# Kernel tuning notes

Measured on AMD Instinct MI355X. Metric: run time of the kernel, lower is better.

The kernel has to match this reference:

```python
import jax, jax.numpy as jnp
import numpy as np

HEADS = 8
LANDMARKS = 256   # dim // 2
PINV_ITERS = 6
CONV_K = 33       # residual_conv_kernel default in NystromAttention
N_BOTTLENECKS = 4
DIM = 512


def layer_norm(x, w, b, eps=1e-5):
    mu = jnp.mean(x, -1, keepdims=True)
    xc = x - mu
    var = jnp.mean(xc * xc, -1, keepdims=True)
    return xc * jax.lax.rsqrt(var + eps) * w + b


def moore_penrose_pinv(x, iters=PINV_ITERS):
    # faithful to lucidrains: global max over row/col sums
    col = jnp.abs(x).sum(-1).max()
    row = jnp.abs(x).sum(-2).max()
    z = jnp.swapaxes(x, -1, -2) / (col * row)
    I = jnp.eye(x.shape[-1], dtype=x.dtype)
    for _ in range(iters):
        xz = x @ z
        z = 0.25 * z @ (13.0 * I - xz @ (15.0 * I - xz @ (7.0 * I - xz)))
    return z


def nystrom_attention(x, qkv_w, out_w, out_b, conv_w):
    b, n, d = x.shape
    m = LANDMARKS
    pad = (-n) % m
    x = jnp.pad(x, ((0, 0), (pad, 0), (0, 0)))  # pad at FRONT of seq, like F.pad
    N = n + pad
    dh = d // HEADS  # 64
    qkv = x @ qkv_w.T                      # (b, N, 3*d)
    q, k, v = jnp.split(qkv, 3, axis=-1)

    def heads(t):
        return t.reshape(b, N, HEADS, dh).transpose(0, 2, 1, 3)  # (b, h, N, dh)

    q, k, v = heads(q), heads(k), heads(v)
    q = q * (dh ** -0.5)
    l = N // m
    # einops reduce '... (n l) d -> ... n d' sum, then / l
    q_l = q.reshape(b, HEADS, m, l, dh).sum(3) / l
    k_l = k.reshape(b, HEADS, m, l, dh).sum(3) / l
    attn1 = jax.nn.softmax(jnp.einsum('bhid,bhjd->bhij', q, k_l), -1)    # (b,h,N,m)
    attn2 = jax.nn.softmax(jnp.einsum('bhid,bhjd->bhij', q_l, k_l), -1)  # (b,h,m,m)
    attn3 = jax.nn.softmax(jnp.einsum('bhid,bhjd->bhij', q_l, k), -1)    # (b,h,m,N)
    attn2_inv = moore_penrose_pinv(attn2)
    out = (attn1 @ attn2_inv) @ (attn3 @ v)  # (b,h,N,dh)
    # residual depthwise conv over seq dim, per head (groups=heads, bias=False)
    res = jax.lax.conv_general_dilated(
        v, conv_w, window_strides=(1, 1),
        padding=((CONV_K // 2, CONV_K // 2), (0, 0)),
        dimension_numbers=('NCHW', 'OIHW', 'NCHW'),
        feature_group_count=HEADS)
    out = out + res
    out = out.transpose(0, 2, 1, 3).reshape(b, N, d)
    out = out @ out_w.T + out_b  # to_out (dropout is identity in eval)
    return out[:, -n:]


def trans_layer(x, ln_w, ln_b, qkv_w, out_w, out_b, conv_w, omega):
    h = layer_norm(x, ln_w, ln_b)
    a = nystrom_attention(h, qkv_w, out_w, out_b, conv_w)
    # torch: `attn_output, *_ = attn(...)` strips batch dim then broadcasts;
    # with b==1 this equals the plain admin residual below.
    return x * omega + a


def setup_inputs() -> dict:
    key = jax.random.key(0)
    ks = jax.random.split(key, 20)
    d = DIM
    s = 1.0 / np.sqrt(d)
    inp = {
        'x1': jax.random.normal(ks[0], (1, 16384, d), jnp.float32),
        'x2': jax.random.normal(ks[1], (1, 2048, d), jnp.float32),
        'bottleneck': jax.random.uniform(ks[2], (1, N_BOTTLENECKS, d), jnp.float32),
    }
    for i, base in ((1, 3), (2, 10)):
        inp[f'ln{i}_w'] = jnp.ones((d,), jnp.float32)
        inp[f'ln{i}_b'] = jnp.zeros((d,), jnp.float32)
        inp[f'qkv{i}_w'] = jax.random.normal(ks[base], (3 * d, d), jnp.float32) * s
        inp[f'out{i}_w'] = jax.random.normal(ks[base + 1], (d, d), jnp.float32) * s
        inp[f'out{i}_b'] = jnp.zeros((d,), jnp.float32)
        inp[f'conv{i}_w'] = jax.random.normal(ks[base + 2], (HEADS, 1, CONV_K, 1), jnp.float32) * (1.0 / np.sqrt(CONV_K))
        inp[f'omega{i}'] = jnp.full((1,), np.sqrt(8.0), jnp.float32)  # admin_torch.as_module(8)
    return inp


def reference(x1, x2, bottleneck,
              ln1_w, ln1_b, qkv1_w, out1_w, out1_b, conv1_w, omega1,
              ln2_w, ln2_b, qkv2_w, out2_w, out2_b, conv2_w, omega2):
    seq = x1.shape[1]
    bn = jnp.concatenate([bottleneck, x2], axis=1)
    bn = trans_layer(bn, ln2_w, ln2_b, qkv2_w, out2_w, out2_b, conv2_w, omega2)
    bn = bn[:, :N_BOTTLENECKS, :]
    x = jnp.concatenate([x1, bn], axis=1)
    x = trans_layer(x, ln1_w, ln1_b, qkv1_w, out1_w, out1_b, conv1_w, omega1)
    return x[:, :seq, :]
```

## Files before the change

kernel.cpp:

```cpp
#include <hip/hip_runtime.h>
#include <math.h>

#define QKVLD 1536

__global__ __launch_bounds__(256) void ln_pad_kernel(
    const float* __restrict__ src1, int n1,
    const float* __restrict__ src2,
    const float* __restrict__ w, const float* __restrict__ b,
    float* __restrict__ h, int pad)
{
    int r = blockIdx.x;
    int tid = threadIdx.x;
    float* out = h + (size_t)r * 512;
    if (r < pad) { out[tid] = 0.f; out[tid + 256] = 0.f; return; }
    int i = r - pad;
    const float* src = (i < n1) ? (src1 + (size_t)i * 512)
                                : (src2 + (size_t)(i - n1) * 512);
    float x0 = src[tid], x1 = src[tid + 256];
    float s = x0 + x1, sq = x0 * x0 + x1 * x1;
#pragma unroll
    for (int o = 32; o >= 1; o >>= 1) { s += __shfl_xor(s, o); sq += __shfl_xor(sq, o); }
    __shared__ float rs[4], rq[4];
    int wid = tid >> 6, lane = tid & 63;
    if (lane == 0) { rs[wid] = s; rq[wid] = sq; }
    __syncthreads();
    s = rs[0] + rs[1] + rs[2] + rs[3];
    sq = rq[0] + rq[1] + rq[2] + rq[3];
    float mu = s * (1.f / 512.f);
    float var = sq * (1.f / 512.f) - mu * mu;
    float inv = rsqrtf(var + 1e-5f);
    out[tid]       = (x0 - mu) * inv * w[tid] + b[tid];
    out[tid + 256] = (x1 - mu) * inv * w[tid + 256] + b[tid + 256];
}

__global__ __launch_bounds__(256) void gemm_nt128(
    const float* __restrict__ A, const float* __restrict__ B, float* __restrict__ C,
    int K, int lda, int ldb, int ldc,
    const float* __restrict__ resid, const float* __restrict__ bias,
    const float* __restrict__ omega)
{
    __shared__ __align__(16) float As[16][128];
    __shared__ __align__(16) float Bs[16][128];
    int tid = threadIdx.x;
    int tx = tid & 15, ty = tid >> 4;
    int row0 = blockIdx.x * 128, col0 = blockIdx.y * 128;
    int lr = tid >> 1, lk = (tid & 1) << 3;
    const float* Ap = A + (size_t)(row0 + lr) * lda + lk;
    const float* Bp = B + (size_t)(col0 + lr) * ldb + lk;
    float acc[8][8] = {};
    float4 a0 = *(const float4*)(Ap);
    float4 a1 = *(const float4*)(Ap + 4);
    float4 b0 = *(const float4*)(Bp);
    float4 b1 = *(const float4*)(Bp + 4);
    for (int kt = 0; kt < K; kt += 16) {
        __syncthreads();
        As[lk + 0][lr] = a0.x; As[lk + 1][lr] = a0.y; As[lk + 2][lr] = a0.z; As[lk + 3][lr] = a0.w;
        As[lk + 4][lr] = a1.x; As[lk + 5][lr] = a1.y; As[lk + 6][lr] = a1.z; As[lk + 7][lr] = a1.w;
        Bs[lk + 0][lr] = b0.x; Bs[lk + 1][lr] = b0.y; Bs[lk + 2][lr] = b0.z; Bs[lk + 3][lr] = b0.w;
        Bs[lk + 4][lr] = b1.x; Bs[lk + 5][lr] = b1.y; Bs[lk + 6][lr] = b1.z; Bs[lk + 7][lr] = b1.w;
        __syncthreads();
        if (kt + 16 < K) {
            a0 = *(const float4*)(Ap + kt + 16); a1 = *(const float4*)(Ap + kt + 20);
            b0 = *(const float4*)(Bp + kt + 16); b1 = *(const float4*)(Bp + kt + 20);
        }
#pragma unroll
        for (int k = 0; k < 16; ++k) {
            float4 av0 = *(const float4*)(&As[k][ty << 2]);
            float4 av1 = *(const float4*)(&As[k][64 + (ty << 2)]);
            float4 bv0 = *(const float4*)(&Bs[k][tx << 2]);
            float4 bv1 = *(const float4*)(&Bs[k][64 + (tx << 2)]);
            float a[8] = {av0.x, av0.y, av0.z, av0.w, av1.x, av1.y, av1.z, av1.w};
            float bb[8] = {bv0.x, bv0.y, bv0.z, bv0.w, bv1.x, bv1.y, bv1.z, bv1.w};
#pragma unroll
            for (int i = 0; i < 8; ++i)
#pragma unroll
                for (int j = 0; j < 8; ++j) acc[i][j] += a[i] * bb[j];
        }
    }
#pragma unroll
    for (int ih = 0; ih < 2; ++ih)
#pragma unroll
    for (int i = 0; i < 4; ++i) {
        int r = row0 + ih * 64 + (ty << 2) + i;
#pragma unroll
        for (int jh = 0; jh < 2; ++jh) {
            int c = col0 + jh * 64 + (tx << 2);
            float4 o = make_float4(acc[ih * 4 + i][jh * 4 + 0], acc[ih * 4 + i][jh * 4 + 1],
                                   acc[ih * 4 + i][jh * 4 + 2], acc[ih * 4 + i][jh * 4 + 3]);
            if (resid) {
                float om = omega[0];
                float4 rv = *(const float4*)(resid + (size_t)r * ldc + c);
                float4 bv = *(const float4*)(bias + c);
                o.x += om * rv.x + bv.x; o.y += om * rv.y + bv.y;
                o.z += om * rv.z + bv.z; o.w += om * rv.w + bv.w;
            }
            *(float4*)(C + (size_t)r * ldc + c) = o;
        }
    }
}

__global__ __launch_bounds__(256) void landmarks_kernel(
    const float* __restrict__ qkv, float* __restrict__ ql, float* __restrict__ kl, int l)
{
    int j = blockIdx.x;
    int tid = threadIdx.x;
    float inv = 1.f / (float)l;
    const float* base = qkv + (size_t)j * l * QKVLD;
    float sq0 = 0, sq1 = 0, sk0 = 0, sk1 = 0;
    for (int r = 0; r < l; ++r) {
        const float* row = base + (size_t)r * QKVLD;
        sq0 += row[tid]; sq1 += row[tid + 256];
        sk0 += row[512 + tid]; sk1 += row[512 + tid + 256];
    }
    ql[j * 512 + tid] = sq0 * inv; ql[j * 512 + tid + 256] = sq1 * inv;
    kl[j * 512 + tid] = sk0 * inv; kl[j * 512 + tid + 256] = sk1 * inv;
}

__global__ __launch_bounds__(256) void attn2_kernel(
    const float* __restrict__ ql, const float* __restrict__ kl, float* __restrict__ a2)
{
    int hh = blockIdx.y, i = blockIdx.x;
    int tid = threadIdx.x;
    __shared__ float qrow[64];
    __shared__ float red[4], red2[4];
    if (tid < 64) qrow[tid] = 0.125f * ql[i * 512 + hh * 64 + tid];
    __syncthreads();
    const float* krow = kl + (size_t)tid * 512 + hh * 64;
    float sc = 0.f;
#pragma unroll
    for (int d = 0; d < 64; ++d) sc += qrow[d] * krow[d];
    float m = sc;
#pragma unroll
    for (int o = 32; o >= 1; o >>= 1) m = fmaxf(m, __shfl_xor(m, o));
    int wid = tid >> 6, lane = tid & 63;
    if (lane == 0) red[wid] = m;
    __syncthreads();
    m = fmaxf(fmaxf(red[0], red[1]), fmaxf(red[2], red[3]));
    float p = __expf(sc - m);
    float s = p;
#pragma unroll
    for (int o = 32; o >= 1; o >>= 1) s += __shfl_xor(s, o);
    if (lane == 0) red2[wid] = s;
    __syncthreads();
    s = red2[0] + red2[1] + red2[2] + red2[3];
    a2[((size_t)hh * 256 + i) * 256 + tid] = p / s;
}

__global__ __launch_bounds__(256) void pinv_norms(const float* __restrict__ x, float* __restrict__ scr)
{
    int hh = blockIdx.x;
    const float* xh = x + ((size_t)hh << 16);
    int tid = threadIdx.x;
    float rs = 0.f, cs = 0.f;
    for (int j = 0; j < 256; ++j) rs += fabsf(xh[tid * 256 + j]);
    for (int i = 0; i < 256; ++i) cs += fabsf(xh[i * 256 + tid]);
#pragma unroll
    for (int o = 32; o >= 1; o >>= 1) { rs = fmaxf(rs, __shfl_xor(rs, o)); cs = fmaxf(cs, __shfl_xor(cs, o)); }
    __shared__ float r4[4], c4[4];
    int wid = tid >> 6, lane = tid & 63;
    if (lane == 0) { r4[wid] = rs; c4[wid] = cs; }
    __syncthreads();
    if (tid == 0) {
        scr[hh]     = fmaxf(fmaxf(r4[0], r4[1]), fmaxf(r4[2], r4[3]));
        scr[8 + hh] = fmaxf(fmaxf(c4[0], c4[1]), fmaxf(c4[2], c4[3]));
    }
}

__global__ __launch_bounds__(256) void pinv_transpose(
    const float* __restrict__ x, const float* __restrict__ scr, float* __restrict__ z)
{
    float col = scr[0], row = scr[8];
#pragma unroll
    for (int k = 1; k < 8; ++k) { col = fmaxf(col, scr[k]); row = fmaxf(row, scr[8 + k]); }
    float s = 1.f / (col * row);
    int idx = blockIdx.x * 256 + threadIdx.x;
    int hh = idx >> 16, rem = idx & 65535, j = rem >> 8, i = rem & 255;
    z[idx] = x[((size_t)hh << 16) + (i << 8) + j] * s;
}

__global__ __launch_bounds__(256) void gemm256_pinv(
    const float* __restrict__ A, const float* __restrict__ B, float* __restrict__ C,
    float alpha, float scl)
{
    int hh = blockIdx.x >> 4, t = blockIdx.x & 15;
    int row0 = (t >> 2) * 64, col0 = (t & 3) * 64;
    const float* Ah = A + ((size_t)hh << 16);
    const float* Bh = B + ((size_t)hh << 16);
    float* Ch = C + ((size_t)hh << 16);
    int tid = threadIdx.x;
    int tx = tid & 15, ty = tid >> 4;
    __shared__ __align__(16) float As[16][64];
    __shared__ __align__(16) float Bs[16][64];
    int lr = tid >> 2, lk = (tid & 3) << 2;
    int bk = tid >> 4, bc = (tid & 15) << 2;
    float acc[4][4] = {};
    float4 a = *(const float4*)(Ah + (size_t)(row0 + lr) * 256 + lk);
    float4 b = *(const float4*)(Bh + (size_t)bk * 256 + col0 + bc);
    for (int kt = 0; kt < 256; kt += 16) {
        __syncthreads();
        As[lk + 0][lr] = a.x; As[lk + 1][lr] = a.y; As[lk + 2][lr] = a.z; As[lk + 3][lr] = a.w;
        *(float4*)(&Bs[bk][bc]) = b;
        __syncthreads();
        if (kt + 16 < 256) {
            a = *(const float4*)(Ah + (size_t)(row0 + lr) * 256 + kt + 16 + lk);
            b = *(const float4*)(Bh + (size_t)(kt + 16 + bk) * 256 + col0 + bc);
        }
#pragma unroll
        for (int k = 0; k < 16; ++k) {
            float4 av = *(const float4*)(&As[k][ty << 2]);
            float4 bv = *(const float4*)(&Bs[k][tx << 2]);
            acc[0][0] += av.x * bv.x; acc[0][1] += av.x * bv.y; acc[0][2] += av.x * bv.z; acc[0][3] += av.x * bv.w;
            acc[1][0] += av.y * bv.x; acc[1][1] += av.y * bv.y; acc[1][2] += av.y * bv.z; acc[1][3] += av.y * bv.w;
            acc[2][0] += av.z * bv.x; acc[2][1] += av.z * bv.y; acc[2][2] += av.z * bv.z; acc[2][3] += av.z * bv.w;
            acc[3][0] += av.w * bv.x; acc[3][1] += av.w * bv.y; acc[3][2] += av.w * bv.z; acc[3][3] += av.w * bv.w;
        }
    }
#pragma unroll
    for (int i = 0; i < 4; ++i) {
        int rr = row0 + (ty << 2) + i, cc = col0 + (tx << 2);
        float4 ae = *(const float4*)(Ah + (size_t)rr * 256 + cc);
        float4 o;
        o.x = scl * (alpha * ae.x - acc[i][0]);
        o.y = scl * (alpha * ae.y - acc[i][1]);
        o.z = scl * (alpha * ae.z - acc[i][2]);
        o.w = scl * (alpha * ae.w - acc[i][3]);
        *(float4*)(Ch + (size_t)rr * 256 + cc) = o;
    }
}

__global__ __launch_bounds__(256) void stage_a(
    const float* __restrict__ qkv, const float* __restrict__ ql, float* __restrict__ av, int N)
{
    int hh = blockIdx.y;
    int q0 = blockIdx.x * 8;
    int tid = threadIdx.x;
    int lane = tid & 63, wid = tid >> 6;
    __shared__ float qs[8][64];
    __shared__ float kv[128 * 65];
    __shared__ float ss[8][128];
    __shared__ float ps[8][128];
    __shared__ float mrow[8], srow[8], scalef[8];
    for (int t = tid; t < 512; t += 256) {
        int r = t >> 6, d = t & 63;
        qs[r][d] = 0.125f * ql[(q0 + r) * 512 + hh * 64 + d];
    }
    if (tid < 8) { mrow[tid] = -1e30f; srow[tid] = 0.f; }
    int d = tid & 63, sub = tid >> 6;
    float acc0 = 0.f, acc1 = 0.f;
    __syncthreads();
    for (int kb = 0; kb < N; kb += 128) {
#pragma unroll
        for (int t = tid; t < 2048; t += 256) {
            int r = t >> 4, d4 = (t & 15) << 2;
            float4 vv = *(const float4*)(&qkv[(size_t)(kb + r) * QKVLD + 512 + hh * 64 + d4]);
            kv[r * 65 + d4 + 0] = vv.x; kv[r * 65 + d4 + 1] = vv.y;
            kv[r * 65 + d4 + 2] = vv.z; kv[r * 65 + d4 + 3] = vv.w;
        }
        __syncthreads();
        {
            int j = tid & 127;
            int rb = (tid >> 7) * 4;
            float s0 = 0, s1 = 0, s2 = 0, s3 = 0;
#pragma unroll
            for (int dd = 0; dd < 64; ++dd) {
                float kvv = kv[j * 65 + dd];
                s0 += qs[rb + 0][dd] * kvv;
                s1 += qs[rb + 1][dd] * kvv;
                s2 += qs[rb + 2][dd] * kvv;
                s3 += qs[rb + 3][dd] * kvv;
            }
            ss[rb + 0][j] = s0; ss[rb + 1][j] = s1; ss[rb + 2][j] = s2; ss[rb + 3][j] = s3;
        }
        __syncthreads();
#pragma unroll
        for (int rr = 0; rr < 2; ++rr) {
            int row = wid + rr * 4;
            float a = ss[row][lane], b2 = ss[row][lane + 64];
            float mx = fmaxf(a, b2);
#pragma unroll
            for (int o = 32; o >= 1; o >>= 1) mx = fmaxf(mx, __shfl_xor(mx, o));
            float newm = fmaxf(mrow[row], mx);
            float pa = __expf(a - newm), pb = __expf(b2 - newm);
            ps[row][lane] = pa; ps[row][lane + 64] = pb;
            float sum = pa + pb;
#pragma unroll
            for (int o = 32; o >= 1; o >>= 1) sum += __shfl_xor(sum, o);
            if (lane == 0) {
                float f = __expf(mrow[row] - newm);
                scalef[row] = f;
                srow[row] = srow[row] * f + sum;
                mrow[row] = newm;
            }
        }
        __syncthreads();
        acc0 *= scalef[sub];
        acc1 *= scalef[sub + 4];
#pragma unroll
        for (int t = tid; t < 2048; t += 256) {
            int r = t >> 4, d4 = (t & 15) << 2;
            float4 vv = *(const float4*)(&qkv[(size_t)(kb + r) * QKVLD + 1024 + hh * 64 + d4]);
            kv[r * 65 + d4 + 0] = vv.x; kv[r * 65 + d4 + 1] = vv.y;
            kv[r * 65 + d4 + 2] = vv.z; kv[r * 65 + d4 + 3] = vv.w;
        }
        __syncthreads();
#pragma unroll 4
        for (int j = 0; j < 128; ++j) {
            float vv = kv[j * 65 + d];
            acc0 += ps[sub][j] * vv;
            acc1 += ps[sub + 4][j] * vv;
        }
        __syncthreads();
    }
    av[((size_t)hh * 256 + q0 + sub) * 64 + d]     = acc0 / srow[sub];
    av[((size_t)hh * 256 + q0 + sub + 4) * 64 + d] = acc1 / srow[sub + 4];
}

__global__ __launch_bounds__(256) void zmm_kernel(
    const float* __restrict__ Z, const float* __restrict__ av, float* __restrict__ t2m)
{
    int hh = blockIdx.y;
    int row0 = blockIdx.x * 64;
    int tid = threadIdx.x;
    int r = tid >> 2, q = tid & 3;
    __shared__ float zs[64][65];
    __shared__ float vs[64][65];
    float acc[16] = {};
#pragma unroll 4
    for (int kc = 0; kc < 4; ++kc) {
        __syncthreads();
        for (int t = tid; t < 4096; t += 256) {
            int a = t >> 6, dd = t & 63;
            zs[a][dd] = Z[((size_t)hh << 16) + (row0 + a) * 256 + kc * 64 + dd];
            vs[a][dd] = av[((size_t)hh * 256 + kc * 64 + a) * 64 + dd];
        }
        __syncthreads();
#pragma unroll
        for (int k = 0; k < 64; ++k) {
            float z = zs[r][k];
#pragma unroll
            for (int dd = 0; dd < 16; ++dd) acc[dd] += z * vs[k][q * 16 + dd];
        }
    }
    float* op = t2m + ((size_t)hh * 256 + row0 + r) * 64 + q * 16;
    *(float4*)(op + 0)  = make_float4(acc[0], acc[1], acc[2], acc[3]);
    *(float4*)(op + 4)  = make_float4(acc[4], acc[5], acc[6], acc[7]);
    *(float4*)(op + 8)  = make_float4(acc[8], acc[9], acc[10], acc[11]);
    *(float4*)(op + 12) = make_float4(acc[12], acc[13], acc[14], acc[15]);
}

__global__ __launch_bounds__(256) void stage_c(
    const float* __restrict__ qkv, const float* __restrict__ kl,
    const float* __restrict__ t2m, float* __restrict__ oh, int r0)
{
    int hh = blockIdx.y;
    int row0 = r0 + blockIdx.x * 64;
    int tid = threadIdx.x;
    int r = tid >> 2, q = tid & 3;
    __shared__ float qs[64][65];
    __shared__ float cs[64][65];
    __shared__ float pl[64][65];
    for (int t = tid; t < 4096; t += 256) {
        int rr = t >> 6, dd = t & 63;
        qs[rr][dd] = 0.125f * qkv[(size_t)(row0 + rr) * QKVLD + hh * 64 + dd];
    }
    float m = -1e30f, l = 0.f;
    float acc[16] = {};
    for (int c = 0; c < 4; ++c) {
        __syncthreads();
        for (int t = tid; t < 4096; t += 256) {
            int jl = t >> 6, dd = t & 63;
            cs[jl][dd] = kl[(c * 64 + jl) * 512 + hh * 64 + dd];
        }
        __syncthreads();
        float s[16];
        float mx = -1e30f;
#pragma unroll
        for (int jj = 0; jj < 16; ++jj) {
            int jl = q * 16 + jj;
            float sv = 0.f;
#pragma unroll
            for (int dd = 0; dd < 64; ++dd) sv += qs[r][dd] * cs[jl][dd];
            s[jj] = sv;
            mx = fmaxf(mx, sv);
        }
        mx = fmaxf(mx, __shfl_xor(mx, 1));
        mx = fmaxf(mx, __shfl_xor(mx, 2));
        float mn = fmaxf(m, mx);
        float scale = __expf(m - mn);
        m = mn;
        float psum = 0.f;
#pragma unroll
        for (int jj = 0; jj < 16; ++jj) { s[jj] = __expf(s[jj] - mn); psum += s[jj]; }
        psum += __shfl_xor(psum, 1);
        psum += __shfl_xor(psum, 2);
        l = l * scale + psum;
#pragma unroll
        for (int i = 0; i < 16; ++i) acc[i] *= scale;
#pragma unroll
        for (int jj = 0; jj < 16; ++jj) pl[r][q * 16 + jj] = s[jj];
        __syncthreads();
        for (int t = tid; t < 4096; t += 256) {
            int jl = t >> 6, dd = t & 63;
            cs[jl][dd] = t2m[((size_t)hh * 256 + c * 64 + jl) * 64 + dd];
        }
        __syncthreads();
#pragma unroll
        for (int j = 0; j < 64; ++j) {
            float p = pl[r][j];
#pragma unroll
            for (int i = 0; i < 16; ++i) acc[i] += p * cs[j][q * 16 + i];
        }
    }
    float invl = 1.f / l;
    float* op = oh + (size_t)(row0 + r) * 512 + hh * 64 + q * 16;
#pragma unroll
    for (int v4 = 0; v4 < 4; ++v4)
        *(float4*)(op + v4 * 4) = make_float4(acc[v4 * 4 + 0] * invl, acc[v4 * 4 + 1] * invl,
                                              acc[v4 * 4 + 2] * invl, acc[v4 * 4 + 3] * invl);
}

__global__ __launch_bounds__(256) void conv_kernel(
    const float* __restrict__ qkv, const float* __restrict__ w,
    float* __restrict__ oh, int r0, int nrows, int N)
{
    int idx = blockIdx.x * 256 + threadIdx.x;
    int nrb = (nrows + 7) >> 3;
    if (idx >= nrb * 512) return;
    int rb = idx >> 9, c = idx & 511;
    int hh = c >> 6;
    int g0 = r0 + rb * 8;
    float wr[33];
#pragma unroll
    for (int k = 0; k < 33; ++k) wr[k] = w[hh * 33 + k];
    float acc[8] = {};
#pragma unroll
    for (int t = 0; t < 41; ++t) {
        int row = g0 + t - 16;
        float v = (row >= 0 && row < N) ? qkv[(size_t)row * QKVLD + 1024 + c] : 0.f;
#pragma unroll
        for (int i = 0; i < 8; ++i) {
            int k = t - i;
            if (k >= 0 && k < 33) acc[i] += wr[k] * v;
        }
    }
#pragma unroll
    for (int i = 0; i < 8; ++i) {
        int g = g0 + i;
        if (g < r0 + nrows) oh[(size_t)g * 512 + c] += acc[i];
    }
}

__global__ __launch_bounds__(256) void l2out_kernel(
    const float* __restrict__ oh, const float* __restrict__ W,
    const float* __restrict__ bias, const float* __restrict__ bott,
    const float* __restrict__ omega, float* __restrict__ bn_new)
{
    int idx = blockIdx.x * 256 + threadIdx.x;
    int i = idx >> 9, j = idx & 511;
    float acc = bias[j];
    const float* ar = oh + (size_t)(252 + i) * 512;
    const float* wr = W + (size_t)j * 512;
    for (int k = 0; k < 512; ++k) acc += ar[k] * wr[k];
    bn_new[idx] = bott[idx] * omega[0] + acc;
}

static void run_layer_common(const float* src1, int n1, const float* src2,
                             const float* lnw, const float* lnb, const float* qkvw,
                             int N, int l,
                             float* h, float* qkv, float* ql, float* kl,
                             float* a2, float* z0, float* z1, float* xz,
                             float* ta, float* tb, float* avb, float* t2m,
                             float* scr, float** z_final, hipStream_t stream)
{
    ln_pad_kernel<<<N, 256, 0, stream>>>(src1, n1, src2, lnw, lnb, h, 252);
    dim3 g1(N / 128, 12);
    gemm_nt128<<<g1, 256, 0, stream>>>(h, qkvw, qkv, 512, 512, 512, QKVLD, nullptr, nullptr, nullptr);
    landmarks_kernel<<<256, 256, 0, stream>>>(qkv, ql, kl, l);
    attn2_kernel<<<dim3(256, 8), 256, 0, stream>>>(ql, kl, a2);
    pinv_norms<<<8, 256, 0, stream>>>(a2, scr);
    pinv_transpose<<<2048, 256, 0, stream>>>(a2, scr, z0);
    float* zc = z0; float* zn = z1;
    for (int it = 0; it < 6; ++it) {
        gemm256_pinv<<<128, 256, 0, stream>>>(a2, zc, xz, 0.f, -1.f);
        gemm256_pinv<<<128, 256, 0, stream>>>(xz, xz, ta, 7.f, 1.f);
        gemm256_pinv<<<128, 256, 0, stream>>>(xz, ta, tb, 15.f, 1.f);
        gemm256_pinv<<<128, 256, 0, stream>>>(zc, tb, zn, 13.f, 0.25f);
        float* tmp = zc; zc = zn; zn = tmp;
    }
    stage_a<<<dim3(32, 8), 256, 0, stream>>>(qkv, ql, avb, N);
    zmm_kernel<<<dim3(4, 8), 256, 0, stream>>>(zc, avb, t2m);
    *z_final = zc;
}

extern "C" void kernel_launch(void* const* d_in, const int* in_sizes, int n_in,
                              void* d_out, int out_size, void* d_ws, size_t ws_size,
                              hipStream_t stream) {
    (void)in_sizes; (void)n_in; (void)out_size; (void)ws_size;
    const float* x1    = (const float*)d_in[0];
    const float* x2    = (const float*)d_in[1];
    const float* bott  = (const float*)d_in[2];
    const float* ln1w  = (const float*)d_in[3];
    const float* ln1b  = (const float*)d_in[4];
    const float* qkv1w = (const float*)d_in[5];
    const float* out1w = (const float*)d_in[6];
    const float* out1b = (const float*)d_in[7];
    const float* cv1w  = (const float*)d_in[8];
    const float* om1   = (const float*)d_in[9];
    const float* ln2w  = (const float*)d_in[10];
    const float* ln2b  = (const float*)d_in[11];
    const float* qkv2w = (const float*)d_in[12];
    const float* out2w = (const float*)d_in[13];
    const float* out2b = (const float*)d_in[14];
    const float* cv2w  = (const float*)d_in[15];
    const float* om2   = (const float*)d_in[16];

    const int N1 = 16640, N2 = 2304;
    float* ws = (float*)d_ws;
    size_t off = 0;
    float* h    = ws + off; off += (size_t)N1 * 512;
    float* oh   = h;
    float* qkv  = ws + off; off += (size_t)N1 * 1536;
    float* ql   = ws + off; off += 256 * 512;
    float* kl   = ws + off; off += 256 * 512;
    float* a2   = ws + off; off += (size_t)8 * 65536;
    float* z0   = ws + off; off += (size_t)8 * 65536;
    float* z1   = ws + off; off += (size_t)8 * 65536;
    float* xz   = ws + off; off += (size_t)8 * 65536;
    float* ta   = ws + off; off += (size_t)8 * 65536;
    float* tb   = ws + off; off += (size_t)8 * 65536;
    float* avb  = ws + off; off += (size_t)8 * 256 * 64;
    float* t2m  = ws + off; off += (size_t)8 * 256 * 64;
    float* bnn  = ws + off; off += 4 * 512;
    float* scr  = ws + off; off += 64;

    float* zf = nullptr;

    run_layer_common(bott, 4, x2, ln2w, ln2b, qkv2w, N2, 9,
                     h, qkv, ql, kl, a2, z0, z1, xz, ta, tb, avb, t2m, scr, &zf, stream);
    stage_c<<<dim3(1, 8), 256, 0, stream>>>(qkv, kl, t2m, oh, 252);
    {
        int nrb = 1, thr = nrb * 512;
        conv_kernel<<<(thr + 255) / 256, 256, 0, stream>>>(qkv, cv2w, oh, 252, 4, N2);
    }
    l2out_kernel<<<8, 256, 0, stream>>>(oh, out2w, out2b, bott, om2, bnn);

    run_layer_common(x1, 16384, bnn, ln1w, ln1b, qkv1w, N1, 65,
                     h, qkv, ql, kl, a2, z0, z1, xz, ta, tb, avb, t2m, scr, &zf, stream);
    stage_c<<<dim3(256, 8), 256, 0, stream>>>(qkv, kl, t2m, oh, 252);
    {
        int nrb = 16384 / 8, thr = nrb * 512;
        conv_kernel<<<(thr + 255) / 256, 256, 0, stream>>>(qkv, cv1w, oh, 252, 16384, N1);
    }
    dim3 g2(16384 / 128, 4);
    gemm_nt128<<<g2, 256, 0, stream>>>(oh + (size_t)252 * 512, out1w, (float*)d_out,
                                       512, 512, 512, 512, x1, out1b, om1);
}
```

Before: 4.136 ms.

## Split stage_a over key chunks with combine pass; retile pinv GEMM smaller

The landmark-query attention over all keys (stage_a) now runs as split-K: eight slices each process a range of key blocks and write partial accumulators plus running max and sum. A combine kernel then merges them with log-sum-exp rescaling, raising the grid from 256 blocks to 2048 for the long second layer. Shared-memory reads in stage_a are vectorised with float4 using padded stride 68. The 256x256 pinv GEMM moves to 32x64 tiles with a k-step of 64, doubling its block count. The split adds workspace traffic and an extra launch.

```diff
diff --git a/kernel.cpp b/kernel.cpp
--- a/kernel.cpp
+++ b/kernel.cpp
@@ -182,63 +182,77 @@
     const float* __restrict__ A, const float* __restrict__ B, float* __restrict__ C,
     float alpha, float scl)
 {
-    int hh = blockIdx.x >> 4, t = blockIdx.x & 15;
-    int row0 = (t >> 2) * 64, col0 = (t & 3) * 64;
+    int hh = blockIdx.x >> 5, t = blockIdx.x & 31;
+    int row0 = (t >> 2) << 5, col0 = (t & 3) << 6;
     const float* Ah = A + ((size_t)hh << 16);
     const float* Bh = B + ((size_t)hh << 16);
     float* Ch = C + ((size_t)hh << 16);
     int tid = threadIdx.x;
-    int tx = tid & 15, ty = tid >> 4;
-    __shared__ __align__(16) float As[16][64];
-    __shared__ __align__(16) float Bs[16][64];
-    int lr = tid >> 2, lk = (tid & 3) << 2;
-    int bk = tid >> 4, bc = (tid & 15) << 2;
-    float acc[4][4] = {};
-    float4 a = *(const float4*)(Ah + (size_t)(row0 + lr) * 256 + lk);
-    float4 b = *(const float4*)(Bh + (size_t)bk * 256 + col0 + bc);
-    for (int kt = 0; kt < 256; kt += 16) {
-        __syncthreads();
-        As[lk + 0][lr] = a.x; As[lk + 1][lr] = a.y; As[lk + 2][lr] = a.z; As[lk + 3][lr] = a.w;
-        *(float4*)(&Bs[bk][bc]) = b;
-        __syncthreads();
-        if (kt + 16 < 256) {
-            a = *(const float4*)(Ah + (size_t)(row0 + lr) * 256 + kt + 16 + lk);
-            b = *(const float4*)(Bh + (size_t)(kt + 16 + bk) * 256 + col0 + bc);
-        }
-#pragma unroll
-        for (int k = 0; k < 16; ++k) {
-            float4 av = *(const float4*)(&As[k][ty << 2]);
+    __shared__ float As[64][33];
+    __shared__ __align__(16) float Bs[64][68];
+    int alr = tid & 31, alk = (tid >> 5) << 3;
+    int bbk = tid >> 4, bbc = (tid & 15) << 2;
+    int ty = tid >> 4, tx = tid & 15;
+    float acc[2][4] = {};
+    float4 a0 = *(const float4*)(Ah + (size_t)(row0 + alr) * 256 + alk);
+    float4 a1 = *(const float4*)(Ah + (size_t)(row0 + alr) * 256 + alk + 4);
+    float4 bb0 = *(const float4*)(Bh + (size_t)(bbk +  0) * 256 + col0 + bbc);
+    float4 bb1 = *(const float4*)(Bh + (size_t)(bbk + 16) * 256 + col0 + bbc);
+    float4 bb2 = *(const float4*)(Bh + (size_t)(bbk + 32) * 256 + col0 + bbc);
+    float4 bb3 = *(const float4*)(Bh + (size_t)(bbk + 48) * 256 + col0 + bbc);
+    for (int kt = 0; kt < 256; kt += 64) {
+        __syncthreads();
+        As[alk + 0][alr] = a0.x; As[alk + 1][alr] = a0.y; As[alk + 2][alr] = a0.z; As[alk + 3][alr] = a0.w;
+        As[alk + 4][alr] = a1.x; As[alk + 5][alr] = a1.y; As[alk + 6][alr] = a1.z; As[alk + 7][alr] = a1.w;
+        *(float4*)(&Bs[bbk +  0][bbc]) = bb0;
+        *(float4*)(&Bs[bbk + 16][bbc]) = bb1;
+        *(float4*)(&Bs[bbk + 32][bbc]) = bb2;
+        *(float4*)(&Bs[bbk + 48][bbc]) = bb3;
+        __syncthreads();
+        if (kt + 64 < 256) {
+            int kn = kt + 64;
+            a0 = *(const float4*)(Ah + (size_t)(row0 + alr) * 256 + kn + alk);
+            a1 = *(const float4*)(Ah + (size_t)(row0 + alr) * 256 + kn + alk + 4);
+            bb0 = *(const float4*)(Bh + (size_t)(kn + bbk +  0) * 256 + col0 + bbc);
+            bb1 = *(const float4*)(Bh + (size_t)(kn + bbk + 16) * 256 + col0 + bbc);
+            bb2 = *(const float4*)(Bh + (size_t)(kn + bbk + 32) * 256 + col0 + bbc);
+            bb3 = *(const float4*)(Bh + (size_t)(kn + bbk + 48) * 256 + col0 + bbc);
+        }
+#pragma unroll
+        for (int k = 0; k < 64; ++k) {
+            float av0 = As[k][(ty << 1) + 0];
+            float av1 = As[k][(ty << 1) + 1];
             float4 bv = *(const float4*)(&Bs[k][tx << 2]);
-            acc[0][0] += av.x * bv.x; acc[0][1] += av.x * bv.y; acc[0][2] += av.x * bv.z; acc[0][3] += av.x * bv.w;
-            acc[1][0] += av.y * bv.x; acc[1][1] += av.y * bv.y; acc[1][2] += av.y * bv.z; acc[1][3] += av.y * bv.w;
-            acc[2][0] += av.z * bv.x; acc[2][1] += av.z * bv.y; acc[2][2] += av.z * bv.z; acc[2][3] += av.z * bv.w;
-            acc[3][0] += av.w * bv.x; acc[3][1] += av.w * bv.y; acc[3][2] += av.w * bv.z; acc[3][3] += av.w * bv.w;
-        }
-    }
-#pragma unroll
-    for (int i = 0; i < 4; ++i) {
-        int rr = row0 + (ty << 2) + i, cc = col0 + (tx << 2);
+            acc[0][0] += av0 * bv.x; acc[0][1] += av0 * bv.y; acc[0][2] += av0 * bv.z; acc[0][3] += av0 * bv.w;
+            acc[1][0] += av1 * bv.x; acc[1][1] += av1 * bv.y; acc[1][2] += av1 * bv.z; acc[1][3] += av1 * bv.w;
+        }
+    }
+#pragma unroll
+    for (int r = 0; r < 2; ++r) {
+        int rr = row0 + (ty << 1) + r, cc = col0 + (tx << 2);
         float4 ae = *(const float4*)(Ah + (size_t)rr * 256 + cc);
         float4 o;
-        o.x = scl * (alpha * ae.x - acc[i][0]);
-        o.y = scl * (alpha * ae.y - acc[i][1]);
-        o.z = scl * (alpha * ae.z - acc[i][2]);
-        o.w = scl * (alpha * ae.w - acc[i][3]);
+        o.x = scl * (alpha * ae.x - acc[r][0]);
+        o.y = scl * (alpha * ae.y - acc[r][1]);
+        o.z = scl * (alpha * ae.z - acc[r][2]);
+        o.w = scl * (alpha * ae.w - acc[r][3]);
         *(float4*)(Ch + (size_t)rr * 256 + cc) = o;
     }
 }
 
-__global__ __launch_bounds__(256) void stage_a(
-    const float* __restrict__ qkv, const float* __restrict__ ql, float* __restrict__ av, int N)
+__global__ __launch_bounds__(256) void stage_a_slice(
+    const float* __restrict__ qkv, const float* __restrict__ ql,
+    float* __restrict__ pacc, float* __restrict__ pml, int N, int CS)
 {
     int hh = blockIdx.y;
     int q0 = blockIdx.x * 8;
+    int s  = blockIdx.z;
     int tid = threadIdx.x;
     int lane = tid & 63, wid = tid >> 6;
     __shared__ float qs[8][64];
-    __shared__ float kv[128 * 65];
+    __shared__ __align__(16) float kv[128 * 68];
     __shared__ float ss[8][128];
-    __shared__ float ps[8][128];
+    __shared__ __align__(16) float ps[8][128];
     __shared__ float mrow[8], srow[8], scalef[8];
     for (int t = tid; t < 512; t += 256) {
         int r = t >> 6, d = t & 63;
@@ -248,13 +262,15 @@
     int d = tid & 63, sub = tid >> 6;
     float acc0 = 0.f, acc1 = 0.f;
     __syncthreads();
-    for (int kb = 0; kb < N; kb += 128) {
+    int kb0 = s * CS * 128;
+    for (int c = 0; c < CS; ++c) {
+        int kb = kb0 + c * 128;
+        if (kb >= N) break;
 #pragma unroll
         for (int t = tid; t < 2048; t += 256) {
             int r = t >> 4, d4 = (t & 15) << 2;
             float4 vv = *(const float4*)(&qkv[(size_t)(kb + r) * QKVLD + 512 + hh * 64 + d4]);
-            kv[r * 65 + d4 + 0] = vv.x; kv[r * 65 + d4 + 1] = vv.y;
-            kv[r * 65 + d4 + 2] = vv.z; kv[r * 65 + d4 + 3] = vv.w;
+            *(float4*)(&kv[r * 68 + d4]) = vv;
         }
         __syncthreads();
         {
@@ -262,12 +278,16 @@
             int rb = (tid >> 7) * 4;
             float s0 = 0, s1 = 0, s2 = 0, s3 = 0;
 #pragma unroll
-            for (int dd = 0; dd < 64; ++dd) {
-                float kvv = kv[j * 65 + dd];
-                s0 += qs[rb + 0][dd] * kvv;
-                s1 += qs[rb + 1][dd] * kvv;
-                s2 += qs[rb + 2][dd] * kvv;
-                s3 += qs[rb + 3][dd] * kvv;
+            for (int dd4 = 0; dd4 < 64; dd4 += 4) {
+                float4 kvv = *(const float4*)(&kv[j * 68 + dd4]);
+                float4 qv0 = *(const float4*)(&qs[rb + 0][dd4]);
+                float4 qv1 = *(const float4*)(&qs[rb + 1][dd4]);
+                float4 qv2 = *(const float4*)(&qs[rb + 2][dd4]);
+                float4 qv3 = *(const float4*)(&qs[rb + 3][dd4]);
+                s0 += qv0.x * kvv.x + qv0.y * kvv.y + qv0.z * kvv.z + qv0.w * kvv.w;
+                s1 += qv1.x * kvv.x + qv1.y * kvv.y + qv1.z * kvv.z + qv1.w * kvv.w;
+                s2 += qv2.x * kvv.x + qv2.y * kvv.y + qv2.z * kvv.z + qv2.w * kvv.w;
+                s3 += qv3.x * kvv.x + qv3.y * kvv.y + qv3.z * kvv.z + qv3.w * kvv.w;
             }
             ss[rb + 0][j] = s0; ss[rb + 1][j] = s1; ss[rb + 2][j] = s2; ss[rb + 3][j] = s3;
         }
@@ -299,20 +319,53 @@
         for (int t = tid; t < 2048; t += 256) {
             int r = t >> 4, d4 = (t & 15) << 2;
             float4 vv = *(const float4*)(&qkv[(size_t)(kb + r) * QKVLD + 1024 + hh * 64 + d4]);
-            kv[r * 65 + d4 + 0] = vv.x; kv[r * 65 + d4 + 1] = vv.y;
-            kv[r * 65 + d4 + 2] = vv.z; kv[r * 65 + d4 + 3] = vv.w;
-        }
-        __syncthreads();
-#pragma unroll 4
-        for (int j = 0; j < 128; ++j) {
-            float vv = kv[j * 65 + d];
-            acc0 += ps[sub][j] * vv;
-            acc1 += ps[sub + 4][j] * vv;
-        }
-        __syncthreads();
-    }
-    av[((size_t)hh * 256 + q0 + sub) * 64 + d]     = acc0 / srow[sub];
-    av[((size_t)hh * 256 + q0 + sub + 4) * 64 + d] = acc1 / srow[sub + 4];
+            *(float4*)(&kv[r * 68 + d4]) = vv;
+        }
+        __syncthreads();
+#pragma unroll 8
+        for (int j = 0; j < 128; j += 4) {
+            float4 p0 = *(const float4*)(&ps[sub][j]);
+            float4 p1 = *(const float4*)(&ps[sub + 4][j]);
+            float v0 = kv[(j + 0) * 68 + d];
+            float v1 = kv[(j + 1) * 68 + d];
+            float v2 = kv[(j + 2) * 68 + d];
+            float v3 = kv[(j + 3) * 68 + d];
+            acc0 += p0.x * v0 + p0.y * v1 + p0.z * v2 + p0.w * v3;
+            acc1 += p1.x * v0 + p1.y * v1 + p1.z * v2 + p1.w * v3;
+        }
+        __syncthreads();
+    }
+    size_t base0 = (((size_t)hh * 256 + q0 + sub) * 8 + s) * 64 + d;
+    size_t base1 = (((size_t)hh * 256 + q0 + sub + 4) * 8 + s) * 64 + d;
+    pacc[base0] = acc0;
+    pacc[base1] = acc1;
+    if (tid < 8) {
+        size_t mb = (((size_t)hh * 256 + q0 + tid) * 8 + s) * 2;
+        pml[mb] = mrow[tid]; pml[mb + 1] = srow[tid];
+    }
+}
+
+__global__ __launch_bounds__(256) void stage_a_combine(
+    const float* __restrict__ pacc, const float* __restrict__ pml, float* __restrict__ av)
+{
+    int hh = blockIdx.y;
+    int tid = threadIdx.x;
+    int row = blockIdx.x * 4 + (tid >> 6);
+    int d = tid & 63;
+    size_t rb = (size_t)hh * 256 + row;
+    float M = -1e30f;
+#pragma unroll
+    for (int s = 0; s < 8; ++s) M = fmaxf(M, pml[(rb * 8 + s) * 2]);
+    float L = 0.f, a = 0.f;
+#pragma unroll
+    for (int s = 0; s < 8; ++s) {
+        float ms = pml[(rb * 8 + s) * 2];
+        float ls = pml[(rb * 8 + s) * 2 + 1];
+        float f = __expf(ms - M);
+        L += ls * f;
+        a += pacc[(rb * 8 + s) * 64 + d] * f;
+    }
+    av[rb * 64 + d] = a / L;
 }
 
 __global__ __launch_bounds__(256) void zmm_kernel(
@@ -470,6 +523,7 @@
                              float* h, float* qkv, float* ql, float* kl,
                              float* a2, float* z0, float* z1, float* xz,
                              float* ta, float* tb, float* avb, float* t2m,
+                             float* pacc, float* pml,
                              float* scr, float** z_final, hipStream_t stream)
 {
     ln_pad_kernel<<<N, 256, 0, stream>>>(src1, n1, src2, lnw, lnb, h, 252);
@@ -481,13 +535,15 @@
     pinv_transpose<<<2048, 256, 0, stream>>>(a2, scr, z0);
     float* zc = z0; float* zn = z1;
     for (int it = 0; it < 6; ++it) {
-        gemm256_pinv<<<128, 256, 0, stream>>>(a2, zc, xz, 0.f, -1.f);
-        gemm256_pinv<<<128, 256, 0, stream>>>(xz, xz, ta, 7.f, 1.f);
-        gemm256_pinv<<<128, 256, 0, stream>>>(xz, ta, tb, 15.f, 1.f);
-        gemm256_pinv<<<128, 256, 0, stream>>>(zc, tb, zn, 13.f, 0.25f);
+        gemm256_pinv<<<256, 256, 0, stream>>>(a2, zc, xz, 0.f, -1.f);
+        gemm256_pinv<<<256, 256, 0, stream>>>(xz, xz, ta, 7.f, 1.f);
+        gemm256_pinv<<<256, 256, 0, stream>>>(xz, ta, tb, 15.f, 1.f);
+        gemm256_pinv<<<256, 256, 0, stream>>>(zc, tb, zn, 13.f, 0.25f);
         float* tmp = zc; zc = zn; zn = tmp;
     }
-    stage_a<<<dim3(32, 8), 256, 0, stream>>>(qkv, ql, avb, N);
+    int CS = (N / 128 + 7) / 8;
+    stage_a_slice<<<dim3(32, 8, 8), 256, 0, stream>>>(qkv, ql, pacc, pml, N, CS);
+    stage_a_combine<<<dim3(64, 8), 256, 0, stream>>>(pacc, pml, avb);
     zmm_kernel<<<dim3(4, 8), 256, 0, stream>>>(zc, avb, t2m);
     *z_final = zc;
 }
@@ -530,22 +586,21 @@
     float* tb   = ws + off; off += (size_t)8 * 65536;
     float* avb  = ws + off; off += (size_t)8 * 256 * 64;
     float* t2m  = ws + off; off += (size_t)8 * 256 * 64;
+    float* pacc = ws + off; off += (size_t)8 * 256 * 8 * 64;
+    float* pml  = ws + off; off += (size_t)8 * 256 * 8 * 2;
     float* bnn  = ws + off; off += 4 * 512;
     float* scr  = ws + off; off += 64;
 
     float* zf = nullptr;
 
     run_layer_common(bott, 4, x2, ln2w, ln2b, qkv2w, N2, 9,
-                     h, qkv, ql, kl, a2, z0, z1, xz, ta, tb, avb, t2m, scr, &zf, stream);
+                     h, qkv, ql, kl, a2, z0, z1, xz, ta, tb, avb, t2m, pacc, pml, scr, &zf, stream);
     stage_c<<<dim3(1, 8), 256, 0, stream>>>(qkv, kl, t2m, oh, 252);
-    {
-        int nrb = 1, thr = nrb * 512;
-        conv_kernel<<<(thr + 255) / 256, 256, 0, stream>>>(qkv, cv2w, oh, 252, 4, N2);
-    }
+    conv_kernel<<<2, 256, 0, stream>>>(qkv, cv2w, oh, 252, 4, N2);
     l2out_kernel<<<8, 256, 0, stream>>>(oh, out2w, out2b, bott, om2, bnn);
 
     run_layer_common(x1, 16384, bnn, ln1w, ln1b, qkv1w, N1, 65,
-                     h, qkv, ql, kl, a2, z0, z1, xz, ta, tb, avb, t2m, scr, &zf, stream);
+                     h, qkv, ql, kl, a2, z0, z1, xz, ta, tb, avb, t2m, pacc, pml, scr, &zf, stream);
     stage_c<<<dim3(256, 8), 256, 0, stream>>>(qkv, kl, t2m, oh, 252);
     {
         int nrb = 16384 / 8, thr = nrb * 512;
```

Result: faster. 3.345 ms (-19.1%).
